# Optimization experiments

Hardware: AMD Instinct MI355X
Metric: run time of the kernel (lower is better)

The kernel has to match this reference:

```python
import jax, jax.numpy as jnp
from jax import lax
import numpy as np

# Model dims (from MambaVisionEncoder defaults + HF MambaConfig defaults)
HIDDEN = 128      # hidden_dim
DEPTH = 4         # num_hidden_layers
INTER = 4 * HIDDEN  # intermediate_size = 512
STATE = 16        # state_size
DT_RANK = 8       # ceil(hidden/16)
KCONV = 4         # conv_kernel
EPS = 1e-5        # layer_norm_epsilon
B_, T_ = 2, 256
C_, H_, W_ = 3, 224, 224
INPUT_DIM = C_ * H_ * W_


def setup_inputs() -> dict:
    key = jax.random.key(0)
    ks = jax.random.split(key, 8)
    s = 0.02
    return {
        "x": jax.random.normal(ks[0], (B_, T_, C_, H_, W_), jnp.float32),
        # torch Linear weights are [out, in]
        "project_w": jax.random.normal(ks[1], (HIDDEN, INPUT_DIM), jnp.float32) * s,
        "project_b": jnp.zeros((HIDDEN,), jnp.float32),
        "in_proj_w": jax.random.normal(ks[2], (DEPTH, 2 * INTER, HIDDEN), jnp.float32) * s,
        "conv_w": jax.random.normal(ks[3], (DEPTH, INTER, KCONV), jnp.float32) * s,
        "conv_b": jnp.zeros((DEPTH, INTER), jnp.float32),
        "x_proj_w": jax.random.normal(ks[4], (DEPTH, DT_RANK + 2 * STATE, INTER), jnp.float32) * s,
        "dt_proj_w": jax.random.normal(ks[5], (DEPTH, INTER, DT_RANK), jnp.float32) * s,
        "dt_proj_b": jnp.zeros((DEPTH, INTER), jnp.float32),
        # S4D-style init: A_log = log(1..N), broadcast over channels
        "A_log": jnp.log(jnp.broadcast_to(jnp.arange(1, STATE + 1, dtype=jnp.float32), (DEPTH, INTER, STATE))),
        "D_ssm": jnp.ones((DEPTH, INTER), jnp.float32),
        "out_proj_w": jax.random.normal(ks[6], (DEPTH, HIDDEN, INTER), jnp.float32) * s,
        "norm_w": jnp.ones((DEPTH, HIDDEN), jnp.float32),
        "norm_f_w": jnp.ones((HIDDEN,), jnp.float32),
    }


def rmsnorm(x, w):
    var = jnp.mean(jnp.square(x), axis=-1, keepdims=True)
    return x * lax.rsqrt(var + EPS) * w


def mamba_mixer(h, ipw, cw, cb, xpw, dtw, dtb, A_log, Dp, opw):
    # h: [B, T, D]
    Bsz, T, _ = h.shape
    proj = jnp.einsum('btd,ed->bte', h, ipw)          # [B, T, 2I]
    hs, gate = jnp.split(proj, 2, axis=-1)
    hs = hs.transpose(0, 2, 1)                         # [B, I, T]
    # causal depthwise conv1d, kernel KCONV
    conv = lax.conv_general_dilated(
        hs, cw[:, None, :], (1,), [(KCONV - 1, 0)],
        dimension_numbers=('NCH', 'OIH', 'NCH'), feature_group_count=INTER)
    hs = jax.nn.silu(conv + cb[None, :, None])         # [B, I, T]
    ssm_in = jnp.einsum('bit,ei->bte', hs, xpw)        # [B, T, dt_rank+2N]
    dt, Bm, Cm = jnp.split(ssm_in, [DT_RANK, DT_RANK + STATE], axis=-1)
    dt = jax.nn.softplus(jnp.einsum('btr,ir->bti', dt, dtw) + dtb)  # [B, T, I]
    A = -jnp.exp(A_log)                                # [I, N]
    u = hs.transpose(0, 2, 1)                          # [B, T, I]
    dA = jnp.exp(dt[..., None] * A[None, None])        # [B, T, I, N]
    dBu = dt[..., None] * Bm[:, :, None, :] * u[..., None]  # [B, T, I, N]

    def step(state, inp):                              # state: [B, I, N]
        dA_t, dBu_t, C_t = inp
        state = dA_t * state + dBu_t
        y_t = jnp.einsum('bin,bn->bi', state, C_t)
        return state, y_t

    init = jnp.zeros((Bsz, INTER, STATE), hs.dtype)
    _, ys = lax.scan(step, init, (dA.transpose(1, 0, 2, 3), dBu.transpose(1, 0, 2, 3), Cm.transpose(1, 0, 2)))
    y = ys.transpose(1, 0, 2)                          # [B, T, I]
    y = (y + u * Dp[None, None, :]) * jax.nn.silu(gate)
    return jnp.einsum('bti,di->btd', y, opw)           # [B, T, D]


def reference(x, project_w, project_b, in_proj_w, conv_w, conv_b, x_proj_w,
              dt_proj_w, dt_proj_b, A_log, D_ssm, out_proj_w, norm_w, norm_f_w):
    B, T = x.shape[0], x.shape[1]
    flat = x.reshape(B, T, -1)                         # [B, T, input_dim]
    h = jnp.einsum('bti,di->btd', flat, project_w) + project_b  # [B, T, HIDDEN]
    for l in range(DEPTH):
        h = h + mamba_mixer(rmsnorm(h, norm_w[l]), in_proj_w[l], conv_w[l], conv_b[l],
                            x_proj_w[l], dt_proj_w[l], dt_proj_b[l], A_log[l],
                            D_ssm[l], out_proj_w[l])
    return rmsnorm(h, norm_f_w)
```

## Files before the change

### kernel.cpp

```cpp
#include <hip/hip_runtime.h>
#include <hip/hip_bf16.h>

#define HIDDEN 128
#define DEPTH 4
#define INTER 512
#define NSTATE 16
#define DT_RANK 8
#define EPS_RMS 1e-5f
#define MTOK 512
#define KIN 150528

typedef __attribute__((ext_vector_type(8))) short bf16x8;
typedef __attribute__((ext_vector_type(4))) float f32x4;

__device__ __forceinline__ unsigned short f2bf(float f) {
  unsigned int u = __builtin_bit_cast(unsigned int, f);
  u += 0x7fffu + ((u >> 16) & 1u);
  return (unsigned short)(u >> 16);
}
__device__ __forceinline__ float silu_f(float x) {
  return x / (1.0f + __expf(-x));
}

__global__ __launch_bounds__(256) void zero_part(float* __restrict__ p)
{
  const size_t i = (size_t)blockIdx.x * 256 + threadIdx.x;
  ((float4*)p)[i] = (float4){0.f, 0.f, 0.f, 0.f};
}

__global__ __launch_bounds__(512) void proj_gemm(
    const float* __restrict__ x, const float* __restrict__ w,
    float* __restrict__ partial)
{
  const int bid = blockIdx.x;
  const int mb = (bid >> 3) & 3;
  const int kb = (bid & 7) + (bid >> 5) * 8;
  const int nchunk = 18 + (kb < 24 ? 1 : 0);
  const int c0 = kb * 18 + (kb < 24 ? kb : 24);

  __shared__ char sm[256 * 256];

  const int tid = threadIdx.x;
  const int lane = tid & 63;
  const int wv = tid >> 6;
  const int wm2 = wv >> 2;
  const int wn4 = wv & 3;
  const int fr = lane & 15;
  const int kq = lane >> 4;
  const int l31 = lane & 31;
  const int rpar = lane >> 5;

  const float* gptr = (wv < 4)
      ? (x + (size_t)(mb * 128 + wv * 32 + rpar) * KIN + l31 * 4)
      : (w + (size_t)((wv - 4) * 32 + rpar) * KIN + l31 * 4);

  f32x4 acc[4][2];
  #pragma unroll
  for (int mi = 0; mi < 4; ++mi) {
    acc[mi][0] = (f32x4){0.f, 0.f, 0.f, 0.f};
    acc[mi][1] = (f32x4){0.f, 0.f, 0.f, 0.f};
  }

  float4 rv[16];
  {
    const float* base = gptr + (size_t)c0 * 128;
    #pragma unroll
    for (int j = 0; j < 16; ++j)
      rv[j] = *(const float4*)(base + (size_t)(j * 2) * KIN);
  }

  for (int cc = 0; cc < nchunk; ++cc) {
    #pragma unroll
    for (int j = 0; j < 16; ++j) {
      const int r = wv * 32 + j * 2 + rpar;
      const int phys = (l31 * 8) ^ ((r & 7) << 4);
      ushort4 bq = {f2bf(rv[j].x), f2bf(rv[j].y), f2bf(rv[j].z), f2bf(rv[j].w)};
      *(ushort4*)(sm + r * 256 + phys) = bq;
    }
    __syncthreads();
    if (cc + 1 < nchunk) {
      const float* base = gptr + (size_t)(c0 + cc + 1) * 128;
      #pragma unroll
      for (int j = 0; j < 16; ++j)
        rv[j] = *(const float4*)(base + (size_t)(j * 2) * KIN);
    }
    #pragma unroll
    for (int ks = 0; ks < 4; ++ks) {
      const int log = ks * 64 + kq * 16;
      bf16x8 a[4];
      #pragma unroll
      for (int mi = 0; mi < 4; ++mi) {
        const int row = wm2 * 64 + mi * 16 + fr;
        a[mi] = *(const bf16x8*)(sm + row * 256 + (log ^ ((row & 7) << 4)));
      }
      #pragma unroll
      for (int ni = 0; ni < 2; ++ni) {
        const int row = 128 + wn4 * 32 + ni * 16 + fr;
        const bf16x8 b = *(const bf16x8*)(sm + row * 256 + (log ^ ((row & 7) << 4)));
        #pragma unroll
        for (int mi = 0; mi < 4; ++mi)
          acc[mi][ni] = __builtin_amdgcn_mfma_f32_16x16x32_bf16(a[mi], b, acc[mi][ni], 0, 0, 0);
      }
    }
    __syncthreads();
  }
  float* hp = partial + (size_t)(kb & 15) * (MTOK * HIDDEN);
  #pragma unroll
  for (int mi = 0; mi < 4; ++mi)
    #pragma unroll
    for (int ni = 0; ni < 2; ++ni)
      #pragma unroll
      for (int r = 0; r < 4; ++r) {
        const int row = mb * 128 + wm2 * 64 + mi * 16 + kq * 4 + r;
        const int col = wn4 * 32 + ni * 16 + fr;
        atomicAdd(hp + (size_t)row * HIDDEN + col, acc[mi][ni][r]);
      }
}

__global__ __launch_bounds__(512) void fusedA(
    int mode,
    const float* __restrict__ part, const float* __restrict__ pb,
    const float* __restrict__ yT, const float* __restrict__ gate_g,
    float* __restrict__ h_g,
    const float* __restrict__ opw,
    const float* __restrict__ nw,
    const float* __restrict__ ipw,
    float* __restrict__ hs_g, float* __restrict__ gate_out,
    float* __restrict__ dout)
{
  const int m0 = blockIdx.x * 2;
  const int tid = threadIdx.x;
  const int o2 = tid >> 1;
  const int half = tid & 1;
  const int t = o2 >> 7, d = o2 & 127;
  __shared__ float y2[2][512];
  __shared__ float hrow[2][128];
  __shared__ float hn[2][128];

  float hv;
  if (mode == 0) {
    hv = pb[d];
    #pragma unroll
    for (int s = 0; s < 16; ++s)
      hv += part[(size_t)s * (MTOK * HIDDEN) + (size_t)(m0 + t) * 128 + d];
  } else {
    #pragma unroll
    for (int j = 0; j < 2; ++j) {
      const int o = tid + j * 512;
      const int tt = o >> 9, i = o & 511;
      const int gt = m0 + tt;
      const int b = gt >> 8, tb = gt & 255;
      const float yv = yT[((size_t)b * 512 + i) * 256 + tb];
      const float g  = gate_g[(size_t)gt * 512 + i];
      y2[tt][i] = yv * silu_f(g);
    }
    __syncthreads();
    const float4* yp = (const float4*)(&y2[t][0] + half * 256);
    const float4* wp = (const float4*)(opw + (size_t)d * 512 + half * 256);
    float a0 = 0.f, a1 = 0.f, a2 = 0.f, a3 = 0.f;
    #pragma unroll 8
    for (int kk = 0; kk < 64; ++kk) {
      const float4 yv = yp[kk], wv4 = wp[kk];
      a0 += yv.x * wv4.x; a1 += yv.y * wv4.y;
      a2 += yv.z * wv4.z; a3 += yv.w * wv4.w;
    }
    float a = (a0 + a1) + (a2 + a3);
    a += __shfl_xor(a, 1);
    hv = h_g[(size_t)(m0 + t) * 128 + d] + a;
  }
  if (mode != 2 && half == 0) h_g[(size_t)(m0 + t) * 128 + d] = hv;
  if (half == 0) hrow[t][d] = hv;
  __syncthreads();
  {
    const int wvi = tid >> 6, ln = tid & 63;
    const int tt = wvi & 1;
    const float v0 = hrow[tt][ln], v1 = hrow[tt][ln + 64];
    float ss = v0 * v0 + v1 * v1;
    #pragma unroll
    for (int off = 1; off < 64; off <<= 1) ss += __shfl_xor(ss, off);
    const float rr = rsqrtf(ss * (1.0f / 128.0f) + EPS_RMS);
    if (mode == 2) {
      if (wvi < 2) {
        dout[(size_t)(m0 + tt) * 128 + ln]      = v0 * rr * nw[ln];
        dout[(size_t)(m0 + tt) * 128 + ln + 64] = v1 * rr * nw[ln + 64];
      }
      return;
    }
    if (wvi < 2) {
      hn[tt][ln]      = v0 * rr * nw[ln];
      hn[tt][ln + 64] = v1 * rr * nw[ln + 64];
    }
  }
  __syncthreads();
  #pragma unroll
  for (int j = 0; j < 4; ++j) {
    const int o = tid + j * 512;
    const int tt = o >> 10, e = o & 1023;
    const float4* hp4 = (const float4*)&hn[tt][0];
    const float4* wp4 = (const float4*)(ipw + (size_t)e * 128);
    float a0 = 0.f, a1 = 0.f, a2 = 0.f, a3 = 0.f;
    #pragma unroll
    for (int kk = 0; kk < 32; ++kk) {
      const float4 hvv = hp4[kk], wv4 = wp4[kk];
      a0 += hvv.x * wv4.x; a1 += hvv.y * wv4.y;
      a2 += hvv.z * wv4.z; a3 += hvv.w * wv4.w;
    }
    const float a = (a0 + a1) + (a2 + a3);
    if (e < 512) hs_g[(size_t)(m0 + tt) * 512 + e] = a;
    else         gate_out[(size_t)(m0 + tt) * 512 + (e - 512)] = a;
  }
}

__global__ __launch_bounds__(512) void convxp(
    const float* __restrict__ hs_g, const float* __restrict__ cw,
    const float* __restrict__ cb, const float* __restrict__ xpw,
    const float* __restrict__ dtw, const float* __restrict__ dtb,
    float* __restrict__ uG, float* __restrict__ dtG,
    float* __restrict__ Bm, float* __restrict__ Cm)
{
  const int m0 = blockIdx.x * 2;
  const int b = m0 >> 8, tb0 = m0 & 255;
  const int tid = threadIdx.x;
  __shared__ float hs5[5][512];
  __shared__ float u4[2][512];
  __shared__ float si[2][40];
  for (int o = tid; o < 2560; o += 512) {
    const int j = o >> 9, i = o & 511;
    const int ct = tb0 - 3 + j;
    hs5[j][i] = (ct >= 0) ? hs_g[((size_t)b * 256 + ct) * 512 + i] : 0.f;
  }
  __syncthreads();
  #pragma unroll
  for (int j = 0; j < 2; ++j) {
    const int o = tid + j * 512;
    const int t = o >> 9, i = o & 511;
    const float4 c4v = *(const float4*)(cw + (size_t)i * 4);
    const float s = cb[i] + c4v.x * hs5[t][i] + c4v.y * hs5[t + 1][i]
                          + c4v.z * hs5[t + 2][i] + c4v.w * hs5[t + 3][i];
    const float uu = silu_f(s);
    u4[t][i] = uu;
    uG[((size_t)b * 256 + tb0 + t) * 512 + i] = uu;
  }
  __syncthreads();
  if (tid < 160) {
    const int pid = tid >> 1, half = tid & 1;
    const int t = pid / 40, e = pid % 40;
    const float4* up = (const float4*)(&u4[t][0] + half * 256);
    const float4* wp = (const float4*)(xpw + (size_t)e * 512 + half * 256);
    float a0 = 0.f, a1 = 0.f, a2 = 0.f, a3 = 0.f;
    #pragma unroll 8
    for (int kk = 0; kk < 64; ++kk) {
      const float4 uv = up[kk], wv4 = wp[kk];
      a0 += uv.x * wv4.x; a1 += uv.y * wv4.y;
      a2 += uv.z * wv4.z; a3 += uv.w * wv4.w;
    }
    float a = (a0 + a1) + (a2 + a3);
    a += __shfl_xor(a, 1);
    if (half == 0) si[t][e] = a;
  }
  __syncthreads();
  if (tid < 64) {
    const int t = tid >> 5, q = tid & 31;
    if (q < 16) Bm[(size_t)(m0 + t) * 16 + q] = si[t][8 + q];
    else        Cm[(size_t)(m0 + t) * 16 + (q - 16)] = si[t][24 + (q - 16)];
  }
  #pragma unroll
  for (int j = 0; j < 2; ++j) {
    const int o = tid + j * 512;
    const int t = o >> 9, i = o & 511;
    float a0 = dtb[i];
    const float* dr = dtw + (size_t)i * 8;
    #pragma unroll
    for (int r = 0; r < 8; ++r) a0 += si[t][r] * dr[r];
    const float sp = (a0 > 20.f) ? a0 : log1pf(__expf(a0));
    dtG[((size_t)b * 256 + tb0 + t) * 512 + i] = sp;
  }
}

__global__ __launch_bounds__(256) void scan_k(
    const float* __restrict__ uG, const float* __restrict__ dtG,
    const float* __restrict__ Bm, const float* __restrict__ Cm,
    const float* __restrict__ Alog, const float* __restrict__ Dssm,
    float* __restrict__ yT)
{
  const int blk = blockIdx.x;
  const int b = blk >> 9, i = blk & 511;
  const int tid = threadIdx.x;
  __shared__ float dt_r[256], u_r[256];
  __shared__ float B_l[256][17], C_l[256][17];
  __shared__ float e_l[16][17], P_l[16][17];
  dt_r[tid] = dtG[((size_t)b * 256 + tid) * 512 + i];
  u_r[tid]  = uG [((size_t)b * 256 + tid) * 512 + i];
  #pragma unroll
  for (int j = 0; j < 16; ++j) {
    const int o = tid + j * 256;
    B_l[o >> 4][o & 15] = Bm[(size_t)b * 4096 + o];
    C_l[o >> 4][o & 15] = Cm[(size_t)b * 4096 + o];
  }
  __syncthreads();
  const int c = tid >> 4, n = tid & 15;
  const float Av = -__expf(Alog[(size_t)i * 16 + n]);
  const float Dv = Dssm[i];
  float aj[16], xj[16];
  float s = 0.f, P = 1.f;
  #pragma unroll
  for (int j = 0; j < 16; ++j) {
    const int t = c * 16 + j;
    const float dtv = dt_r[t];
    const float a = __expf(Av * dtv);
    const float xx = dtv * B_l[t][n] * u_r[t];
    aj[j] = a; xj[j] = xx;
    s = a * s + xx; P *= a;
  }
  e_l[c][n] = s; P_l[c][n] = P;
  __syncthreads();
  float s0 = 0.f;
  for (int cc = 0; cc < c; ++cc)
    s0 = P_l[cc][n] * s0 + e_l[cc][n];
  s = s0;
  #pragma unroll
  for (int j = 0; j < 16; ++j) {
    const int t = c * 16 + j;
    s = aj[j] * s + xj[j];
    float p = s * C_l[t][n];
    p += __shfl_xor(p, 1); p += __shfl_xor(p, 2);
    p += __shfl_xor(p, 4); p += __shfl_xor(p, 8);
    if (n == 0)
      yT[((size_t)b * 512 + i) * 256 + t] = p + u_r[t] * Dv;
  }
}

extern "C" void kernel_launch(void* const* d_in, const int* in_sizes, int n_in,
                              void* d_out, int out_size, void* d_ws, size_t ws_size,
                              hipStream_t stream)
{
  (void)in_sizes; (void)n_in; (void)out_size; (void)ws_size;
  const float* x    = (const float*)d_in[0];
  const float* pw   = (const float*)d_in[1];
  const float* pb   = (const float*)d_in[2];
  const float* ipw  = (const float*)d_in[3];
  const float* cw   = (const float*)d_in[4];
  const float* cb   = (const float*)d_in[5];
  const float* xpw  = (const float*)d_in[6];
  const float* dtw  = (const float*)d_in[7];
  const float* dtb  = (const float*)d_in[8];
  const float* Alog = (const float*)d_in[9];
  const float* Dssm = (const float*)d_in[10];
  const float* opw  = (const float*)d_in[11];
  const float* nw   = (const float*)d_in[12];
  const float* nwf  = (const float*)d_in[13];
  float* out = (float*)d_out;

  float* ws   = (float*)d_ws;
  float* part = ws;
  float* h    = part + 16 * 65536;
  float* hs   = h + 65536;
  float* gate = hs + 262144;
  float* uG   = gate + 262144;
  float* dtG  = uG + 262144;
  float* Bm   = dtG + 262144;
  float* Cm   = Bm + 8192;
  float* yT   = Cm + 8192;

  zero_part<<<dim3(1024), 256, 0, stream>>>(part);
  proj_gemm<<<dim3(256), 512, 0, stream>>>(x, pw, part);

  fusedA<<<dim3(256), 512, 0, stream>>>(0, part, pb, nullptr, nullptr, h,
                                        nullptr, nw, ipw, hs, gate, nullptr);
  for (int l = 0; l < DEPTH; ++l) {
    convxp<<<dim3(256), 512, 0, stream>>>(
        hs, cw + (size_t)l * 2048, cb + (size_t)l * 512,
        xpw + (size_t)l * 40 * 512, dtw + (size_t)l * 512 * 8,
        dtb + (size_t)l * 512, uG, dtG, Bm, Cm);
    scan_k<<<dim3(1024), 256, 0, stream>>>(
        uG, dtG, Bm, Cm, Alog + (size_t)l * 512 * 16, Dssm + (size_t)l * 512, yT);
    if (l < DEPTH - 1)
      fusedA<<<dim3(256), 512, 0, stream>>>(1, nullptr, nullptr, yT, gate, h,
          opw + (size_t)l * 128 * 512, nw + (size_t)(l + 1) * 128,
          ipw + (size_t)(l + 1) * 1024 * 128, hs, gate, nullptr);
    else
      fusedA<<<dim3(256), 512, 0, stream>>>(2, nullptr, nullptr, yT, gate, h,
          opw + (size_t)l * 128 * 512, nwf, nullptr, nullptr, nullptr, out);
  }
}
```

Before: 416.4 us.

## Fuse out_proj/in_proj kernel with conv and x_proj via halo recompute

Merges the per-layer fusedA and convxp kernels into one kernel. Each block recomputes the three previous timesteps of the residual, RMSNorm and in_proj as a causal-conv halo, so the hs tensor never goes to global memory. h and gate are double-buffered so that blocks reading neighbouring rows do not race with writers. This removes one launch and one global round trip of hs per layer, at the cost of 2.5x redundant out_proj/in_proj arithmetic on the hs half.

New measurement: 632.8 us. 1.52x slower.

```diff
diff --git a/kernel.cpp b/kernel.cpp
--- a/kernel.cpp
+++ b/kernel.cpp
@@ -20,6 +20,9 @@
 }
 __device__ __forceinline__ float silu_f(float x) {
   return x / (1.0f + __expf(-x));
+}
+__device__ __forceinline__ float f4sum(f32x4 v) {
+  return (v.x + v.y) + (v.z + v.w);
 }
 
 __global__ __launch_bounds__(256) void zero_part(float* __restrict__ p)
@@ -117,15 +120,178 @@
       }
 }
 
-__global__ __launch_bounds__(512) void fusedA(
+__global__ __launch_bounds__(512) void fconv(
     int mode,
     const float* __restrict__ part, const float* __restrict__ pb,
-    const float* __restrict__ yT, const float* __restrict__ gate_g,
-    float* __restrict__ h_g,
+    const float* __restrict__ yT, const float* __restrict__ gin,
+    const float* __restrict__ hin, float* __restrict__ hout,
+    float* __restrict__ gout,
     const float* __restrict__ opw,
     const float* __restrict__ nw,
     const float* __restrict__ ipw,
-    float* __restrict__ hs_g, float* __restrict__ gate_out,
+    const float* __restrict__ cw, const float* __restrict__ cb,
+    const float* __restrict__ xpw,
+    const float* __restrict__ dtw, const float* __restrict__ dtb,
+    float* __restrict__ uG, float* __restrict__ dtG,
+    float* __restrict__ Bm, float* __restrict__ Cm)
+{
+  const int m0 = blockIdx.x * 2;
+  const int b = m0 >> 8, tb0 = m0 & 255;
+  const int tid = threadIdx.x;
+
+  __shared__ float y2hs[5 * 512];
+  __shared__ float hrow[5 * 128];
+  __shared__ float hn[5 * 128];
+  __shared__ float u_loc[2 * 512];
+  __shared__ float si[2 * 40];
+
+  if (mode == 0) {
+    for (int o = tid; o < 640; o += 512) {
+      const int j = o >> 7, d = o & 127;
+      const int wt = tb0 - 3 + j;
+      float hv = 0.f;
+      if (wt >= 0) {
+        const int gt = b * 256 + wt;
+        hv = pb[d];
+        #pragma unroll
+        for (int s = 0; s < 16; ++s)
+          hv += part[(size_t)s * (MTOK * HIDDEN) + (size_t)gt * 128 + d];
+        if (j >= 3) hout[(size_t)gt * 128 + d] = hv;
+      }
+      hrow[j * 128 + d] = hv;
+    }
+  } else {
+    for (int o = tid; o < 2560; o += 512) {
+      const int j = o >> 9, i = o & 511;
+      const int wt = tb0 - 3 + j;
+      float v = 0.f;
+      if (wt >= 0) {
+        const int gt = b * 256 + wt;
+        v = yT[((size_t)b * 512 + i) * 256 + wt] *
+            silu_f(gin[(size_t)gt * 512 + i]);
+      }
+      y2hs[j * 512 + i] = v;
+    }
+    __syncthreads();
+    {
+      const int d = tid >> 2, kq = tid & 3;
+      const f32x4* wp = (const f32x4*)(opw + (size_t)d * 512 + kq * 128);
+      f32x4 acc[5];
+      #pragma unroll
+      for (int j = 0; j < 5; ++j) acc[j] = (f32x4){0.f, 0.f, 0.f, 0.f};
+      #pragma unroll
+      for (int kk = 0; kk < 32; ++kk) {
+        const f32x4 wv4 = wp[kk];
+        #pragma unroll
+        for (int j = 0; j < 5; ++j)
+          acc[j] += ((const f32x4*)(y2hs + j * 512 + kq * 128))[kk] * wv4;
+      }
+      #pragma unroll
+      for (int j = 0; j < 5; ++j) {
+        float a = f4sum(acc[j]);
+        a += __shfl_xor(a, 1); a += __shfl_xor(a, 2);
+        if (kq == 0) {
+          const int wt = tb0 - 3 + j;
+          if (wt >= 0) {
+            const int gt = b * 256 + wt;
+            const float hv = hin[(size_t)gt * 128 + d] + a;
+            hrow[j * 128 + d] = hv;
+            if (j >= 3) hout[(size_t)gt * 128 + d] = hv;
+          } else hrow[j * 128 + d] = 0.f;
+        }
+      }
+    }
+  }
+  __syncthreads();
+  {
+    const int wv = tid >> 6, ln = tid & 63;
+    if (wv < 5) {
+      const float v0 = hrow[wv * 128 + ln], v1 = hrow[wv * 128 + ln + 64];
+      float ss = v0 * v0 + v1 * v1;
+      #pragma unroll
+      for (int off = 1; off < 64; off <<= 1) ss += __shfl_xor(ss, off);
+      const float rr = rsqrtf(ss * (1.0f / 128.0f) + EPS_RMS);
+      hn[wv * 128 + ln]      = v0 * rr * nw[ln];
+      hn[wv * 128 + ln + 64] = v1 * rr * nw[ln + 64];
+    }
+  }
+  __syncthreads();
+  #pragma unroll
+  for (int jj = 0; jj < 2; ++jj) {
+    const int e = tid + jj * 512;
+    const f32x4* wp4 = (const f32x4*)(ipw + (size_t)e * 128);
+    f32x4 acc[5];
+    #pragma unroll
+    for (int j = 0; j < 5; ++j) acc[j] = (f32x4){0.f, 0.f, 0.f, 0.f};
+    #pragma unroll
+    for (int kk = 0; kk < 32; ++kk) {
+      const f32x4 wv4 = wp4[kk];
+      #pragma unroll
+      for (int j = 0; j < 5; ++j)
+        acc[j] += ((const f32x4*)(hn + j * 128))[kk] * wv4;
+    }
+    if (jj == 0) {
+      #pragma unroll
+      for (int j = 0; j < 5; ++j) y2hs[j * 512 + tid] = f4sum(acc[j]);
+    } else {
+      gout[(size_t)m0 * 512 + tid]       = f4sum(acc[3]);
+      gout[(size_t)(m0 + 1) * 512 + tid] = f4sum(acc[4]);
+    }
+  }
+  __syncthreads();
+  #pragma unroll
+  for (int jj = 0; jj < 2; ++jj) {
+    const int o = tid + jj * 512;
+    const int t = o >> 9, i = o & 511;
+    const float4 c4v = *(const float4*)(cw + (size_t)i * 4);
+    const float s = cb[i] + c4v.x * y2hs[t * 512 + i]
+                          + c4v.y * y2hs[(t + 1) * 512 + i]
+                          + c4v.z * y2hs[(t + 2) * 512 + i]
+                          + c4v.w * y2hs[(t + 3) * 512 + i];
+    const float uu = silu_f(s);
+    u_loc[t * 512 + i] = uu;
+    uG[((size_t)b * 256 + tb0 + t) * 512 + i] = uu;
+  }
+  __syncthreads();
+  if (tid < 160) {
+    const int pid = tid >> 1, half = tid & 1;
+    const int t = pid / 40, e = pid % 40;
+    const float4* up = (const float4*)(u_loc + t * 512 + half * 256);
+    const float4* wp = (const float4*)(xpw + (size_t)e * 512 + half * 256);
+    float a0 = 0.f, a1 = 0.f, a2 = 0.f, a3 = 0.f;
+    #pragma unroll 8
+    for (int kk = 0; kk < 64; ++kk) {
+      const float4 uv = up[kk], wv4 = wp[kk];
+      a0 += uv.x * wv4.x; a1 += uv.y * wv4.y;
+      a2 += uv.z * wv4.z; a3 += uv.w * wv4.w;
+    }
+    float a = (a0 + a1) + (a2 + a3);
+    a += __shfl_xor(a, 1);
+    if (half == 0) si[t * 40 + e] = a;
+  }
+  __syncthreads();
+  if (tid < 64) {
+    const int t = tid >> 5, q = tid & 31;
+    if (q < 16) Bm[(size_t)(m0 + t) * 16 + q] = si[t * 40 + 8 + q];
+    else        Cm[(size_t)(m0 + t) * 16 + (q - 16)] = si[t * 40 + 24 + (q - 16)];
+  }
+  #pragma unroll
+  for (int jj = 0; jj < 2; ++jj) {
+    const int o = tid + jj * 512;
+    const int t = o >> 9, i = o & 511;
+    float a0 = dtb[i];
+    const float* dr = dtw + (size_t)i * 8;
+    #pragma unroll
+    for (int r = 0; r < 8; ++r) a0 += si[t * 40 + r] * dr[r];
+    const float sp = (a0 > 20.f) ? a0 : log1pf(__expf(a0));
+    dtG[((size_t)b * 256 + tb0 + t) * 512 + i] = sp;
+  }
+}
+
+__global__ __launch_bounds__(512) void fafin(
+    const float* __restrict__ yT, const float* __restrict__ gin,
+    const float* __restrict__ hin,
+    const float* __restrict__ opw, const float* __restrict__ nwf,
     float* __restrict__ dout)
 {
   const int m0 = blockIdx.x * 2;
@@ -135,40 +301,30 @@
   const int t = o2 >> 7, d = o2 & 127;
   __shared__ float y2[2][512];
   __shared__ float hrow[2][128];
-  __shared__ float hn[2][128];
-
-  float hv;
-  if (mode == 0) {
-    hv = pb[d];
-    #pragma unroll
-    for (int s = 0; s < 16; ++s)
-      hv += part[(size_t)s * (MTOK * HIDDEN) + (size_t)(m0 + t) * 128 + d];
-  } else {
-    #pragma unroll
-    for (int j = 0; j < 2; ++j) {
-      const int o = tid + j * 512;
-      const int tt = o >> 9, i = o & 511;
-      const int gt = m0 + tt;
-      const int b = gt >> 8, tb = gt & 255;
-      const float yv = yT[((size_t)b * 512 + i) * 256 + tb];
-      const float g  = gate_g[(size_t)gt * 512 + i];
-      y2[tt][i] = yv * silu_f(g);
-    }
-    __syncthreads();
-    const float4* yp = (const float4*)(&y2[t][0] + half * 256);
-    const float4* wp = (const float4*)(opw + (size_t)d * 512 + half * 256);
-    float a0 = 0.f, a1 = 0.f, a2 = 0.f, a3 = 0.f;
-    #pragma unroll 8
-    for (int kk = 0; kk < 64; ++kk) {
-      const float4 yv = yp[kk], wv4 = wp[kk];
-      a0 += yv.x * wv4.x; a1 += yv.y * wv4.y;
-      a2 += yv.z * wv4.z; a3 += yv.w * wv4.w;
-    }
-    float a = (a0 + a1) + (a2 + a3);
-    a += __shfl_xor(a, 1);
-    hv = h_g[(size_t)(m0 + t) * 128 + d] + a;
-  }
-  if (mode != 2 && half == 0) h_g[(size_t)(m0 + t) * 128 + d] = hv;
+
+  #pragma unroll
+  for (int j = 0; j < 2; ++j) {
+    const int o = tid + j * 512;
+    const int tt = o >> 9, i = o & 511;
+    const int gt = m0 + tt;
+    const int b = gt >> 8, tb = gt & 255;
+    const float yv = yT[((size_t)b * 512 + i) * 256 + tb];
+    const float g  = gin[(size_t)gt * 512 + i];
+    y2[tt][i] = yv * silu_f(g);
+  }
+  __syncthreads();
+  const float4* yp = (const float4*)(&y2[t][0] + half * 256);
+  const float4* wp = (const float4*)(opw + (size_t)d * 512 + half * 256);
+  float a0 = 0.f, a1 = 0.f, a2 = 0.f, a3 = 0.f;
+  #pragma unroll 8
+  for (int kk = 0; kk < 64; ++kk) {
+    const float4 yv = yp[kk], wv4 = wp[kk];
+    a0 += yv.x * wv4.x; a1 += yv.y * wv4.y;
+    a2 += yv.z * wv4.z; a3 += yv.w * wv4.w;
+  }
+  float a = (a0 + a1) + (a2 + a3);
+  a += __shfl_xor(a, 1);
+  const float hv = hin[(size_t)(m0 + t) * 128 + d] + a;
   if (half == 0) hrow[t][d] = hv;
   __syncthreads();
   {
@@ -179,101 +335,10 @@
     #pragma unroll
     for (int off = 1; off < 64; off <<= 1) ss += __shfl_xor(ss, off);
     const float rr = rsqrtf(ss * (1.0f / 128.0f) + EPS_RMS);
-    if (mode == 2) {
-      if (wvi < 2) {
-        dout[(size_t)(m0 + tt) * 128 + ln]      = v0 * rr * nw[ln];
-        dout[(size_t)(m0 + tt) * 128 + ln + 64] = v1 * rr * nw[ln + 64];
-      }
-      return;
-    }
     if (wvi < 2) {
-      hn[tt][ln]      = v0 * rr * nw[ln];
-      hn[tt][ln + 64] = v1 * rr * nw[ln + 64];
-    }
-  }
-  __syncthreads();
-  #pragma unroll
-  for (int j = 0; j < 4; ++j) {
-    const int o = tid + j * 512;
-    const int tt = o >> 10, e = o & 1023;
-    const float4* hp4 = (const float4*)&hn[tt][0];
-    const float4* wp4 = (const float4*)(ipw + (size_t)e * 128);
-    float a0 = 0.f, a1 = 0.f, a2 = 0.f, a3 = 0.f;
-    #pragma unroll
-    for (int kk = 0; kk < 32; ++kk) {
-      const float4 hvv = hp4[kk], wv4 = wp4[kk];
-      a0 += hvv.x * wv4.x; a1 += hvv.y * wv4.y;
-      a2 += hvv.z * wv4.z; a3 += hvv.w * wv4.w;
-    }
-    const float a = (a0 + a1) + (a2 + a3);
-    if (e < 512) hs_g[(size_t)(m0 + tt) * 512 + e] = a;
-    else         gate_out[(size_t)(m0 + tt) * 512 + (e - 512)] = a;
-  }
-}
-
-__global__ __launch_bounds__(512) void convxp(
-    const float* __restrict__ hs_g, const float* __restrict__ cw,
-    const float* __restrict__ cb, const float* __restrict__ xpw,
-    const float* __restrict__ dtw, const float* __restrict__ dtb,
-    float* __restrict__ uG, float* __restrict__ dtG,
-    float* __restrict__ Bm, float* __restrict__ Cm)
-{
-  const int m0 = blockIdx.x * 2;
-  const int b = m0 >> 8, tb0 = m0 & 255;
-  const int tid = threadIdx.x;
-  __shared__ float hs5[5][512];
-  __shared__ float u4[2][512];
-  __shared__ float si[2][40];
-  for (int o = tid; o < 2560; o += 512) {
-    const int j = o >> 9, i = o & 511;
-    const int ct = tb0 - 3 + j;
-    hs5[j][i] = (ct >= 0) ? hs_g[((size_t)b * 256 + ct) * 512 + i] : 0.f;
-  }
-  __syncthreads();
-  #pragma unroll
-  for (int j = 0; j < 2; ++j) {
-    const int o = tid + j * 512;
-    const int t = o >> 9, i = o & 511;
-    const float4 c4v = *(const float4*)(cw + (size_t)i * 4);
-    const float s = cb[i] + c4v.x * hs5[t][i] + c4v.y * hs5[t + 1][i]
-                          + c4v.z * hs5[t + 2][i] + c4v.w * hs5[t + 3][i];
-    const float uu = silu_f(s);
-    u4[t][i] = uu;
-    uG[((size_t)b * 256 + tb0 + t) * 512 + i] = uu;
-  }
-  __syncthreads();
-  if (tid < 160) {
-    const int pid = tid >> 1, half = tid & 1;
-    const int t = pid / 40, e = pid % 40;
-    const float4* up = (const float4*)(&u4[t][0] + half * 256);
-    const float4* wp = (const float4*)(xpw + (size_t)e * 512 + half * 256);
-    float a0 = 0.f, a1 = 0.f, a2 = 0.f, a3 = 0.f;
-    #pragma unroll 8
-    for (int kk = 0; kk < 64; ++kk) {
-      const float4 uv = up[kk], wv4 = wp[kk];
-      a0 += uv.x * wv4.x; a1 += uv.y * wv4.y;
-      a2 += uv.z * wv4.z; a3 += uv.w * wv4.w;
-    }
-    float a = (a0 + a1) + (a2 + a3);
-    a += __shfl_xor(a, 1);
-    if (half == 0) si[t][e] = a;
-  }
-  __syncthreads();
-  if (tid < 64) {
-    const int t = tid >> 5, q = tid & 31;
-    if (q < 16) Bm[(size_t)(m0 + t) * 16 + q] = si[t][8 + q];
-    else        Cm[(size_t)(m0 + t) * 16 + (q - 16)] = si[t][24 + (q - 16)];
-  }
-  #pragma unroll
-  for (int j = 0; j < 2; ++j) {
-    const int o = tid + j * 512;
-    const int t = o >> 9, i = o & 511;
-    float a0 = dtb[i];
-    const float* dr = dtw + (size_t)i * 8;
-    #pragma unroll
-    for (int r = 0; r < 8; ++r) a0 += si[t][r] * dr[r];
-    const float sp = (a0 > 20.f) ? a0 : log1pf(__expf(a0));
-    dtG[((size_t)b * 256 + tb0 + t) * 512 + i] = sp;
+      dout[(size_t)(m0 + tt) * 128 + ln]      = v0 * rr * nwf[ln];
+      dout[(size_t)(m0 + tt) * 128 + ln + 64] = v1 * rr * nwf[ln + 64];
+    }
   }
 }
 
@@ -353,10 +418,11 @@
 
   float* ws   = (float*)d_ws;
   float* part = ws;
-  float* h    = part + 16 * 65536;
-  float* hs   = h + 65536;
-  float* gate = hs + 262144;
-  float* uG   = gate + 262144;
+  float* hA   = part + 16 * 65536;
+  float* hB   = hA + 65536;
+  float* gA   = hB + 65536;
+  float* gB   = gA + 262144;
+  float* uG   = gB + 262144;
   float* dtG  = uG + 262144;
   float* Bm   = dtG + 262144;
   float* Cm   = Bm + 8192;
@@ -365,21 +431,31 @@
   zero_part<<<dim3(1024), 256, 0, stream>>>(part);
   proj_gemm<<<dim3(256), 512, 0, stream>>>(x, pw, part);
 
-  fusedA<<<dim3(256), 512, 0, stream>>>(0, part, pb, nullptr, nullptr, h,
-                                        nullptr, nw, ipw, hs, gate, nullptr);
+  fconv<<<dim3(256), 512, 0, stream>>>(
+      0, part, pb, nullptr, nullptr, nullptr, hA, gA,
+      nullptr, nw, ipw,
+      cw, cb, xpw, dtw, dtb, uG, dtG, Bm, Cm);
+
   for (int l = 0; l < DEPTH; ++l) {
-    convxp<<<dim3(256), 512, 0, stream>>>(
-        hs, cw + (size_t)l * 2048, cb + (size_t)l * 512,
-        xpw + (size_t)l * 40 * 512, dtw + (size_t)l * 512 * 8,
-        dtb + (size_t)l * 512, uG, dtG, Bm, Cm);
     scan_k<<<dim3(1024), 256, 0, stream>>>(
         uG, dtG, Bm, Cm, Alog + (size_t)l * 512 * 16, Dssm + (size_t)l * 512, yT);
-    if (l < DEPTH - 1)
-      fusedA<<<dim3(256), 512, 0, stream>>>(1, nullptr, nullptr, yT, gate, h,
-          opw + (size_t)l * 128 * 512, nw + (size_t)(l + 1) * 128,
-          ipw + (size_t)(l + 1) * 1024 * 128, hs, gate, nullptr);
-    else
-      fusedA<<<dim3(256), 512, 0, stream>>>(2, nullptr, nullptr, yT, gate, h,
-          opw + (size_t)l * 128 * 512, nwf, nullptr, nullptr, nullptr, out);
-  }
-}
+    if (l < DEPTH - 1) {
+      const float* hin  = (l & 1) ? hB : hA;
+      float*       hout = (l & 1) ? hA : hB;
+      const float* gin  = (l & 1) ? gB : gA;
+      float*       gout = (l & 1) ? gA : gB;
+      fconv<<<dim3(256), 512, 0, stream>>>(
+          1, nullptr, nullptr, yT, gin, hin, hout, gout,
+          opw + (size_t)l * 128 * 512,
+          nw + (size_t)(l + 1) * 128,
+          ipw + (size_t)(l + 1) * 1024 * 128,
+          cw + (size_t)(l + 1) * 2048, cb + (size_t)(l + 1) * 512,
+          xpw + (size_t)(l + 1) * 40 * 512,
+          dtw + (size_t)(l + 1) * 512 * 8, dtb + (size_t)(l + 1) * 512,
+          uG, dtG, Bm, Cm);
+    } else {
+      fafin<<<dim3(256), 512, 0, stream>>>(
+          yT, gB, hB, opw + (size_t)3 * 128 * 512, nwf, out);
+    }
+  }
+}
```
